# Kernel tuning notes

Hardware: AMD Instinct MI355X
Metric: run time of the kernel (lower is better)

The kernel has to match this reference:

```python
import jax, jax.numpy as jnp
import numpy as np

# Config (mirrors CorrLayerDownsample(J=3, L=8, A=1, A_prime=1, M=256, N=256,
# num_channels=1, shift_mode='samec', mask_angles=4)). With samec + 1 channel,
# every pair is 'shifted' (mask index 1) and groups (j1,j2) are contiguous in
# the global moment order, so concatenation reproduces results_storage order.
J, L, A, M, N, NB = 3, 8, 1, 256, 256, 2
MASK_ANGLES = 4
RADII = (1, 2)  # dyadic shift radii (assumed form of create_masks_shift)

def _mask_positions():
    # shift mask 1: origin plus shifts along mask_angles directions at dyadic radii
    pos = {(0, 0)}
    for k in range(MASK_ANGLES):
        th = np.pi * k / MASK_ANGLES
        for r in RADII:
            pos.add((int(round(r * np.cos(th))), int(round(r * np.sin(th)))))
    return sorted(pos)

def _union_flat_idx(h, w):
    # row-major flat indices of the union shift mask at resolution (h, w),
    # matching torch boolean-mask indexing order (mask_downsample + mask_idx_map_1)
    return np.array(sorted(((dx % h) * w + (dy % w)) for dx, dy in _mask_positions()), dtype=np.int64)

UNION_IDX = [_union_flat_idx(M >> j, N >> j) for j in range(J)]
NSHIFT = len(UNION_IDX[0])

# per-(j1,j2) channel gather indices: la = A*L*c + A*l + a = l (A=1, c=0)
# loop order in compute_idx: l1 outer, l2 inner
LA1 = np.repeat(np.arange(L), L)
LA2 = np.tile(np.arange(L), L)

def _spectral_pad(xh, Mn, Nn):
    # zero-pad Fourier representation to (Mn, Nn) -- spectral upsampling
    m, n = xh.shape[-2], xh.shape[-1]
    if (m, n) == (Mn, Nn):
        return xh
    xs = jnp.fft.fftshift(xh, axes=(-2, -1))
    ph, pw = (Mn - m) // 2, (Nn - n) // 2
    pad = [(0, 0)] * (xh.ndim - 2) + [(ph, ph), (pw, pw)]
    xp = jnp.pad(xs, pad)
    return jnp.fft.ifftshift(xp, axes=(-2, -1)) * ((Mn * Nn) / (m * n))

def _forward(xpsi_0, xpsi_1, xpsi_2):
    xs = [xpsi_0, xpsi_1, xpsi_2]
    hats = [jnp.fft.fft2(x.astype(jnp.complex64)) for x in xs]  # [nb, C, h_j, w_j]
    la1 = jnp.asarray(LA1)
    la2 = jnp.asarray(LA2)
    outs = []
    for j1 in range(J):
        h, w = M >> j1, N >> j1
        uidx = jnp.asarray(UNION_IDX[j1])
        h1 = hats[j1][:, la1]  # [nb, P=L*L, h, w]
        for j2 in range(j1, J):
            h2 = hats[j2][:, la2]
            if j2 > j1:
                h2 = _spectral_pad(h2, h, w)  # upsample coarser scale to scale j1
            corr = jnp.fft.ifft2(h1 * jnp.conj(h2)).real  # cross-correlation map
            flat = corr.reshape(corr.shape[0], corr.shape[1], h * w)
            outs.append(flat[:, :, uidx])  # masked downsample: keep shift positions
    return jnp.concatenate(outs, axis=1)  # [nb, total_pairs, NSHIFT]

def setup_inputs():
    key = jax.random.key(0)
    ks = jax.random.split(key, 3)
    return {
        "xpsi_0": jax.random.normal(ks[0], (NB, A * L, M, N), dtype=jnp.float32),
        "xpsi_1": jax.random.normal(ks[1], (NB, A * L, M // 2, N // 2), dtype=jnp.float32),
        "xpsi_2": jax.random.normal(ks[2], (NB, A * L, M // 4, N // 4), dtype=jnp.float32),
    }

def reference(xpsi_0, xpsi_1, xpsi_2):
    return _forward(xpsi_0, xpsi_1, xpsi_2)
```

## Files before the change

### kernel.cpp

```cpp
#include <hip/hip_runtime.h>

#define PI_D 3.14159265358979323846
#define PI_F 3.14159265358979323846f


__device__ inline float rtab_val(int n, int m2, int t) {
  if (t == 0) return 1.0f;
  double th = PI_D * (double)t / (double)n;
  double v = sin(th * (double)(m2 - 1)) / sin(th) + cos(th * (double)m2);
  return (float)(v / (double)m2);
}

__global__ __launch_bounds__(256) void k_front(
    const float* __restrict__ X0, const float* __restrict__ X1,
    const float* __restrict__ X2, float* __restrict__ P1p,
    float* __restrict__ P2p, float* __restrict__ V01, float* __restrict__ V02,
    float* __restrict__ V12, float* __restrict__ T01, float* __restrict__ T02,
    float* __restrict__ T12, float* __restrict__ out) {
  __shared__ float fsm[3840];
  int bid = blockIdx.x;
  int t = threadIdx.x;
  if (bid < 192) {
    const float* X; float* P; int lg, nsp, idx0;
    if (bid < 128) { X = X1; P = P1p; lg = 7; nsp = 8; idx0 = bid; }
    else           { X = X2; P = P2p; lg = 6; nsp = 4; idx0 = bid - 128; }
    int ch = idx0 / nsp, split = idx0 % nsp;
    int n = 1 << lg;
    int total = n * n;
    int chunk = total / nsp;
    int b0 = split * chunk;
    const float* x = X + (size_t)ch * total + b0;
    float s = 0.f;
    for (int i = t; i < chunk; i += 256) {
      int idx = b0 + i;
      float v = x[i];
      s += (((idx >> lg) ^ idx) & 1) ? -v : v;
    }
#pragma unroll
    for (int off = 32; off > 0; off >>= 1) s += __shfl_down(s, off, 64);
    __shared__ float red[4];
    if ((t & 63) == 0) red[t >> 6] = s;
    __syncthreads();
    if (t == 0) P[ch * nsp + split] = red[0] + red[1] + red[2] + red[3];
    return;
  }
  if (bid < 320) {
    int idx = bid - 192;
    int ch = idx >> 3, nxg = (idx & 7) * 16;
    float* Rl = fsm;
    float* Xs = fsm + 256;
    for (int i = t; i < 256; i += 256) Rl[i] = rtab_val(256, 128, i);
    const float4* xch4 =
        (const float4*)(X1 + (size_t)ch * 16384 + (size_t)nxg * 128);
    for (int i = t; i < 512; i += 256) ((float4*)Xs)[i] = xch4[i];
    __syncthreads();
    if (idx == 0)
      for (int i = t; i < 256; i += 256) T01[i] = Rl[i];
    float* vch = V01 + (size_t)ch * 128 * 256;
    for (int i = t; i < 2048; i += 256) {
      int r = i >> 7, k = i & 127;
      vch[(size_t)(nxg + r) * 256 + 2 * k] = Xs[r * 128 + k];
    }
    int cid = t & 63, wq = t >> 6;
    int m0 = 2 * cid + 1, m1 = 2 * cid + 129;
    float acc[4][2];
#pragma unroll
    for (int r = 0; r < 4; ++r) { acc[r][0] = 0.f; acc[r][1] = 0.f; }
    for (int ny = 0; ny < 128; ++ny) {
      float r0 = Rl[(m0 - 2 * ny) & 255];
      float r1 = Rl[(m1 - 2 * ny) & 255];
#pragma unroll
      for (int r = 0; r < 4; ++r) {
        float xv = Xs[(4 * wq + r) * 128 + ny];
        acc[r][0] += xv * r0;
        acc[r][1] += xv * r1;
      }
    }
#pragma unroll
    for (int r = 0; r < 4; ++r) {
      vch[(size_t)(nxg + 4 * wq + r) * 256 + m0] = acc[r][0];
      vch[(size_t)(nxg + 4 * wq + r) * 256 + m1] = acc[r][1];
    }
    return;
  }
  if (bid < 512) {
    int vbid = bid - 320;
    const float* X = X2; float* V;
    int n1, n2, s, ch, nxg, colh;
    if (vbid < 128) {
      V = V02; n1 = 256; n2 = 64; s = 4;
      ch = vbid >> 3; nxg = ((vbid >> 1) & 3) * 16; colh = vbid & 1;
    } else {
      int w = vbid - 128;
      V = V12; n1 = 128; n2 = 64; s = 2;
      ch = w >> 2; nxg = (w & 3) * 16; colh = 0;
    }
    float* Rl = fsm;
    float* Xs = fsm + 256;
    for (int i = t; i < n1; i += 256) Rl[i] = rtab_val(n1, n2, i);
    const float4* xch4 =
        (const float4*)(X + (size_t)ch * n2 * n2 + (size_t)nxg * n2);
    int nx4 = (16 * n2) >> 2;
    for (int i = t; i < nx4; i += 256) ((float4*)Xs)[i] = xch4[i];
    __syncthreads();
    if (vbid == 0)
      for (int i = t; i < 256; i += 256) T02[i] = Rl[i];
    if (vbid == 128)
      for (int i = t; i < 128; i += 256) T12[i] = Rl[i];
    int myq = (t & 63) + colh * 128;
    int nxq = t >> 6;
    int mask = n1 - 1;
    float acc[4][2];
#pragma unroll
    for (int r = 0; r < 4; ++r)
#pragma unroll
      for (int c = 0; c < 2; ++c) acc[r][c] = 0.f;
    for (int ny = 0; ny < n2; ++ny) {
      float xv[4];
#pragma unroll
      for (int r = 0; r < 4; ++r) xv[r] = Xs[(4 * nxq + r) * n2 + ny];
#pragma unroll
      for (int c = 0; c < 2; ++c) {
        float rv = Rl[(myq + 64 * c - s * ny) & mask];
#pragma unroll
        for (int r = 0; r < 4; ++r) acc[r][c] += xv[r] * rv;
      }
    }
    float* vch = V + (size_t)ch * n2 * n1;
#pragma unroll
    for (int r = 0; r < 4; ++r)
      for (int c = 0; c < 2; ++c)
        vch[(size_t)(nxg + 4 * nxq + r) * n1 + myq + 64 * c] = acc[r][c];
    return;
  }
  int lane = t & 63;
  int wv = t >> 6;
  float accC[8][7];
#pragma unroll
  for (int i = 0; i < 8; ++i)
#pragma unroll
    for (int p = 0; p < 7; ++p) accC[i][p] = 0.f;
  int w = bid - 512;
  const float* Ab; int loc, lgn1, lgc, base;
  if (w < 256)      { loc = w;       Ab = X0; lgn1 = 8; lgc = 4; base = 0;   }
  else if (w < 384) { loc = w - 256; Ab = X1; lgn1 = 7; lgc = 3; base = 192; }
  else              { loc = w - 384; Ab = X2; lgn1 = 6; lgc = 2; base = 320; }
  int n1 = 1 << lgn1;
  int mask = n1 - 1;
  int n1sq = n1 * n1;
  int chunk = loc & ((1 << lgc) - 1);
  int bl2 = loc >> lgc;
  int b = bl2 >> 3, l2 = bl2 & 7;
  const float* A1 = Ab + (size_t)(b * 8) * n1sq;
  const float* A2 = Ab + (size_t)(b * 8 + l2) * n1sq;
  int lgtpr = lgn1 - 2;
  int tpr = 1 << lgtpr;
  int rif = 256 >> lgtpr;
  int rid = t >> lgtpr;
  int cid2 = t & (tpr - 1);
  int ty = cid2 * 4;
  int tym = (ty - 4) & mask;
  for (int rr = 0; rr < 16; rr += rif) {
    int row = chunk * 16 + rr + rid;
    const float* r0 = A2 + (size_t)row * n1;
    const float* r1 = A2 + (size_t)((row - 1) & mask) * n1;
    const float* r2 = A2 + (size_t)((row - 2) & mask) * n1;
    const float* r3 = A2 + (size_t)((row + 1) & mask) * n1;
    float4 a0 = *(const float4*)(r0 + tym);
    float4 b0 = *(const float4*)(r0 + ty);
    float4 a1 = *(const float4*)(r1 + tym);
    float4 b1 = *(const float4*)(r1 + ty);
    float4 b2 = *(const float4*)(r2 + ty);
    float4 a3 = *(const float4*)(r3 + tym);
    float4 b3 = *(const float4*)(r3 + ty);
    const float* rA = A1 + (size_t)row * n1 + ty;
#pragma unroll
    for (int l1 = 0; l1 < 8; ++l1) {
      float4 xv = *(const float4*)(rA + (size_t)l1 * n1sq);
      accC[l1][0] += xv.x * b0.x + xv.y * b0.y + xv.z * b0.z + xv.w * b0.w;
      accC[l1][1] += xv.x * a0.w + xv.y * b0.x + xv.z * b0.y + xv.w * b0.z;
      accC[l1][2] += xv.x * a0.z + xv.y * a0.w + xv.z * b0.x + xv.w * b0.y;
      accC[l1][3] += xv.x * b1.x + xv.y * b1.y + xv.z * b1.z + xv.w * b1.w;
      accC[l1][4] += xv.x * a1.w + xv.y * b1.x + xv.z * b1.y + xv.w * b1.z;
      accC[l1][5] += xv.x * b2.x + xv.y * b2.y + xv.z * b2.z + xv.w * b2.w;
      accC[l1][6] += xv.x * a3.w + xv.y * b3.x + xv.z * b3.y + xv.w * b3.z;
    }
  }
  float* sh = fsm;
  float* af = &accC[0][0];
#pragma unroll
  for (int j = 0; j < 56; ++j) {
    float v = af[j];
    v += __shfl_down(v, 32, 64);
    v += __shfl_down(v, 16, 64);
    af[j] = v;
  }
  __syncthreads();
  if (lane < 16) {
    float* rowp = sh + (wv * 16 + lane) * 60;
#pragma unroll
    for (int j = 0; j < 14; ++j)
      *(float4*)&rowp[4 * j] =
          make_float4(af[4 * j], af[4 * j + 1], af[4 * j + 2], af[4 * j + 3]);
  }
  __syncthreads();
  if (t < 224) {
    int v = t >> 2, q = t & 3;
    float s2 = 0.f;
#pragma unroll
    for (int i = 0; i < 16; ++i) s2 += sh[(q * 16 + i) * 60 + v];
    s2 += __shfl_down(s2, 2, 64);
    s2 += __shfl_down(s2, 1, 64);
    if (q == 0) {
      int l1o = v / 7, p = v % 7;
      atomicAdd(&out[((size_t)b * 384 + base + l1o * 8 + l2) * 7 + p], s2);
    }
  }
}

__global__ __launch_bounds__(256) void k_main(const float* __restrict__ X0,
                                              const float* __restrict__ X1,
                                              const float* __restrict__ V01,
                                              const float* __restrict__ V02,
                                              const float* __restrict__ V12,
                                              const float* __restrict__ P1p,
                                              const float* __restrict__ P2p,
                                              const float* __restrict__ T01,
                                              const float* __restrict__ T02,
                                              const float* __restrict__ T12,
                                              float* __restrict__ out) {
  __shared__ float sRl[256];
  __shared__ float sh[4864];
  __shared__ float Vs[2][2048];
  int u = blockIdx.x;
  int t = threadIdx.x;
  int lane = t & 63;
  int wv = t >> 6;

  const float* V; const float* Pp; const float* A1b; const float* T;
  int n1, n2, s, ch, chunk, nsp, lgn1, base; float inv;
  if (u < 256) {
    V = V01; Pp = P1p; nsp = 8; A1b = X0; n1 = 256; n2 = 128; s = 2;
    inv = 1.f / 16384.f; ch = u >> 4; chunk = u & 15; lgn1 = 8; base = 64;
    T = T01;
  } else if (u < 512) {
    int w = u - 256;
    V = V02; Pp = P2p; nsp = 4; A1b = X0; n1 = 256; n2 = 64; s = 4;
    inv = 1.f / 4096.f; ch = w >> 4; chunk = w & 15; lgn1 = 8; base = 128;
    T = T02;
  } else {
    int w = u - 512;
    V = V12; Pp = P2p; nsp = 4; A1b = X1; n1 = 128; n2 = 64; s = 2;
    inv = 1.f / 4096.f; ch = w >> 3; chunk = w & 7; lgn1 = 7; base = 256;
    T = T12;
  }
  int mask = n1 - 1;
  for (int i = t; i < n1; i += 256) sRl[i] = T[i];
  int mxg = chunk * 16;
  int b = ch >> 3, l2 = ch & 7;
  const float* vch = V + (size_t)ch * n2 * n1;
  float Pv = 0.f;
  for (int i = 0; i < nsp; ++i) Pv += Pp[ch * nsp + i];
  float a = PI_F / (float)s;
  int per = 2 * s;

  if (n1 == 256) {
    if (s == 2) {
      for (int i = t; i < 640; i += 256) {
        int rl = 2 * (i >> 6), c4 = (i & 63) * 4;
        int mx = (mxg - 2 + rl) & 255;
        *(float4*)&sh[rl * 256 + c4] =
            *(const float4*)(vch + (size_t)(mx >> 1) * 256 + c4);
      }
    } else {
      for (int i = t; i < 320; i += 256) {
        int rl = 2 + 4 * (i >> 6), c4 = (i & 63) * 4;
        int mx = (mxg - 2 + rl) & 255;
        *(float4*)&sh[rl * 256 + c4] =
            *(const float4*)(vch + (size_t)(mx >> 2) * 256 + c4);
      }
    }
  } else {
    for (int i = t; i < 320; i += 256) {
      int rl = 2 * (i >> 5), c4 = (i & 31) * 4;
      int mx = (mxg - 2 + rl) & 127;
      *(float4*)&sh[rl * 128 + c4] =
          *(const float4*)(vch + (size_t)(mx >> 1) * 128 + c4);
    }
  }

  int nr, rls[4];
  if (s == 2) {
    if (wv == 0)      { nr = 3; rls[0] = 1;  rls[1] = 3;  rls[2] = 5;  rls[3] = 1; }
    else if (wv == 1) { nr = 2; rls[0] = 7;  rls[1] = 9;  rls[2] = 7;  rls[3] = 7; }
    else if (wv == 2) { nr = 2; rls[0] = 11; rls[1] = 13; rls[2] = 11; rls[3] = 11; }
    else              { nr = 2; rls[0] = 15; rls[1] = 17; rls[2] = 15; rls[3] = 15; }
  } else {
    if (wv == 0)      { nr = 4; rls[0] = 0;  rls[1] = 1;  rls[2] = 3;  rls[3] = 4; }
    else if (wv == 1) { nr = 4; rls[0] = 5;  rls[1] = 7;  rls[2] = 8;  rls[3] = 9; }
    else if (wv == 2) { nr = 3; rls[0] = 11; rls[1] = 12; rls[2] = 13; rls[3] = 11; }
    else              { nr = 3; rls[0] = 15; rls[1] = 16; rls[2] = 17; rls[3] = 15; }
  }
  int bj[4];
#pragma unroll
  for (int j = 0; j < 4; ++j) bj[j] = (mxg - 2 + rls[j]) & mask;

  const float4* vp4 = (const float4*)vch;
  if (n1 == 256) {
    int ntl = n2 >> 3;
    for (int i = t; i < 512; i += 256) ((float4*)Vs[0])[i] = vp4[i];
    __syncthreads();
    float4 acc[4];
#pragma unroll
    for (int j = 0; j < 4; ++j) acc[j] = make_float4(0.f, 0.f, 0.f, 0.f);
    for (int tl = 0; tl < ntl; ++tl) {
      float4 stg0, stg1;
      bool has = (tl + 1 < ntl);
      if (has) {
        stg0 = vp4[(size_t)(tl + 1) * 512 + t];
        stg1 = vp4[(size_t)(tl + 1) * 512 + 256 + t];
      }
      const float* Vc = Vs[tl & 1];
      int tb = tl * 8;
#pragma unroll
      for (int kk = 0; kk < 8; ++kk) {
        float4 vv = *(const float4*)&Vc[kk * 256 + 4 * lane];
        int ss = s * (tb + kk);
#pragma unroll
        for (int j = 0; j < 4; ++j)
          if (j < nr) {
            float rv = sRl[(bj[j] - ss) & 255];
            acc[j].x += rv * vv.x;
            acc[j].y += rv * vv.y;
            acc[j].z += rv * vv.z;
            acc[j].w += rv * vv.w;
          }
      }
      if (has) {
        float4* d = (float4*)Vs[(tl & 1) ^ 1];
        d[t] = stg0;
        d[256 + t] = stg1;
      }
      __syncthreads();
    }
    float smy[4];
#pragma unroll
    for (int j = 0; j < 4; ++j)
      smy[j] = sinf(a * (float)((4 * lane + j) & (per - 1)));
#pragma unroll
    for (int j = 0; j < 4; ++j)
      if (j < nr) {
        float q = inv * sinf(a * (float)(bj[j] & (per - 1))) * Pv;
        float4 o = acc[j];
        o.x -= q * smy[0];
        o.y -= q * smy[1];
        o.z -= q * smy[2];
        o.w -= q * smy[3];
        *(float4*)&sh[rls[j] * 256 + 4 * lane] = o;
      }
  } else {
    for (int i = t; i < 256; i += 256) ((float4*)Vs[0])[i] = vp4[i];
    __syncthreads();
    float2 acc[4];
#pragma unroll
    for (int j = 0; j < 4; ++j) acc[j] = make_float2(0.f, 0.f);
    for (int tl = 0; tl < 8; ++tl) {
      float4 stg0;
      bool has = (tl + 1 < 8);
      if (has) stg0 = vp4[(size_t)(tl + 1) * 256 + t];
      const float* Vc = Vs[tl & 1];
      int tb = tl * 8;
#pragma unroll
      for (int kk = 0; kk < 8; ++kk) {
        float2 vv = *(const float2*)&Vc[kk * 128 + 2 * lane];
        int ss = 2 * (tb + kk);
#pragma unroll
        for (int j = 0; j < 4; ++j)
          if (j < nr) {
            float rv = sRl[(bj[j] - ss) & 127];
            acc[j].x += rv * vv.x;
            acc[j].y += rv * vv.y;
          }
      }
      if (has) ((float4*)Vs[(tl & 1) ^ 1])[t] = stg0;
      __syncthreads();
    }
    const float a2 = PI_F * 0.5f;
    float smy0 = sinf(a2 * (float)((2 * lane) & 3));
    float smy1 = sinf(a2 * (float)((2 * lane + 1) & 3));
#pragma unroll
    for (int j = 0; j < 4; ++j)
      if (j < nr) {
        float q = inv * sinf(a2 * (float)(bj[j] & 3)) * Pv;
        float2 o = acc[j];
        o.x -= q * smy0;
        o.y -= q * smy1;
        *(float2*)&sh[rls[j] * 128 + 2 * lane] = o;
      }
  }
  __syncthreads();

  float accC[8][7];
#pragma unroll
  for (int i = 0; i < 8; ++i)
#pragma unroll
    for (int p = 0; p < 7; ++p) accC[i][p] = 0.f;
  int lgtpr = lgn1 - 2;
  int tpr = 1 << lgtpr;
  int rif = 256 >> lgtpr;
  int rid = t >> lgtpr;
  int cid2 = t & (tpr - 1);
  int ty = cid2 * 4;
  int tym = (ty - 4) & mask;
  int n1sq = n1 * n1;
  const float* A1 = A1b + (size_t)(b * 8) * n1sq;
  for (int rr = 0; rr < 16; rr += rif) {
    int ri = rr + rid;
    const float* r0 = &sh[(ri + 2) * n1];
    const float* r1 = &sh[(ri + 1) * n1];
    const float* r2 = &sh[ri * n1];
    const float* r3 = &sh[(ri + 3) * n1];
    float4 a0 = *(const float4*)(r0 + tym);
    float4 b0 = *(const float4*)(r0 + ty);
    float4 a1 = *(const float4*)(r1 + tym);
    float4 b1 = *(const float4*)(r1 + ty);
    float4 b2 = *(const float4*)(r2 + ty);
    float4 a3 = *(const float4*)(r3 + tym);
    float4 b3 = *(const float4*)(r3 + ty);
    const float* rA = A1 + (size_t)(mxg + ri) * n1 + ty;
#pragma unroll
    for (int l1 = 0; l1 < 8; ++l1) {
      float4 xv = *(const float4*)(rA + (size_t)l1 * n1sq);
      accC[l1][0] += xv.x * b0.x + xv.y * b0.y + xv.z * b0.z + xv.w * b0.w;
      accC[l1][1] += xv.x * a0.w + xv.y * b0.x + xv.z * b0.y + xv.w * b0.z;
      accC[l1][2] += xv.x * a0.z + xv.y * a0.w + xv.z * b0.x + xv.w * b0.y;
      accC[l1][3] += xv.x * b1.x + xv.y * b1.y + xv.z * b1.z + xv.w * b1.w;
      accC[l1][4] += xv.x * a1.w + xv.y * b1.x + xv.z * b1.y + xv.w * b1.z;
      accC[l1][5] += xv.x * b2.x + xv.y * b2.y + xv.z * b2.z + xv.w * b2.w;
      accC[l1][6] += xv.x * a3.w + xv.y * b3.x + xv.z * b3.y + xv.w * b3.z;
    }
  }

  float* af = &accC[0][0];
#pragma unroll
  for (int j = 0; j < 56; ++j) {
    float v = af[j];
    v += __shfl_down(v, 32, 64);
    v += __shfl_down(v, 16, 64);
    af[j] = v;
  }
  __syncthreads();
  if (lane < 16) {
    float* rowp = sh + (wv * 16 + lane) * 60;
#pragma unroll
    for (int j = 0; j < 14; ++j)
      *(float4*)&rowp[4 * j] =
          make_float4(af[4 * j], af[4 * j + 1], af[4 * j + 2], af[4 * j + 3]);
  }
  __syncthreads();
  if (t < 224) {
    int v = t >> 2, q = t & 3;
    float s2 = 0.f;
#pragma unroll
    for (int i = 0; i < 16; ++i) s2 += sh[(q * 16 + i) * 60 + v];
    s2 += __shfl_down(s2, 2, 64);
    s2 += __shfl_down(s2, 1, 64);
    if (q == 0) {
      int l1o = v / 7, p = v % 7;
      atomicAdd(&out[((size_t)b * 384 + base + l1o * 8 + l2) * 7 + p], s2);
    }
  }
}

extern "C" void kernel_launch(void* const* d_in, const int* in_sizes, int n_in,
                              void* d_out, int out_size, void* d_ws, size_t ws_size,
                              hipStream_t stream) {
  const float* X0 = (const float*)d_in[0];
  const float* X1 = (const float*)d_in[1];
  const float* X2 = (const float*)d_in[2];
  float* out = (float*)d_out;
  float* ws = (float*)d_ws;

  float* V01 = ws + 2359296;
  float* V02 = ws + 2883584;
  float* V12 = ws + 3145728;
  float* P1p = ws + 3276800;
  float* P2p = ws + 3276928;
  float* T01 = ws + 3276992;
  float* T02 = ws + 3277248;
  float* T12 = ws + 3277504;

  hipMemsetAsync(d_out, 0, (size_t)out_size, stream);
  k_front<<<960, 256, 0, stream>>>(X0, X1, X2, P1p, P2p, V01, V02, V12, T01,
                                   T02, T12, out);
  k_main<<<640, 256, 0, stream>>>(X0, X1, V01, V02, V12, P1p, P2p, T01, T02,
                                  T12, out);
}
```

Measured before the change: 96.27 us.

## Move same-scale correlation blocks into main kernel and zero output in-kernel

The same-scale direct-correlation blocks (448 of them) move from the front kernel into the main kernel, which grows from 640 to 1088 blocks. The front kernel shrinks to the V/P precompute plus one extra block that zeroes the output buffer, replacing the separate hipMemsetAsync. This drops one memset launch and shortens the critical-path front kernel, and the front kernel's shared buffer shrinks. The risk is a heavier, more register-hungry main kernel and less overlap between the independent correlation work and the precompute stage.

Result: slower. 107.2 us (+11.4%).

```diff
diff --git a/kernel.cpp b/kernel.cpp
--- a/kernel.cpp
+++ b/kernel.cpp
@@ -17,9 +17,13 @@
     float* __restrict__ P2p, float* __restrict__ V01, float* __restrict__ V02,
     float* __restrict__ V12, float* __restrict__ T01, float* __restrict__ T02,
     float* __restrict__ T12, float* __restrict__ out) {
-  __shared__ float fsm[3840];
+  __shared__ float fsm[2304];
   int bid = blockIdx.x;
   int t = threadIdx.x;
+  if (bid == 512) {
+    for (int i = t; i < 5376; i += 256) out[i] = 0.f;
+    return;
+  }
   if (bid < 192) {
     const float* X; float* P; int lg, nsp, idx0;
     if (bid < 128) { X = X1; P = P1p; lg = 7; nsp = 8; idx0 = bid; }
@@ -83,7 +87,7 @@
     }
     return;
   }
-  if (bid < 512) {
+  {
     int vbid = bid - 320;
     const float* X = X2; float* V;
     int n1, n2, s, ch, nxg, colh;
@@ -131,95 +135,12 @@
     for (int r = 0; r < 4; ++r)
       for (int c = 0; c < 2; ++c)
         vch[(size_t)(nxg + 4 * nxq + r) * n1 + myq + 64 * c] = acc[r][c];
-    return;
-  }
-  int lane = t & 63;
-  int wv = t >> 6;
-  float accC[8][7];
-#pragma unroll
-  for (int i = 0; i < 8; ++i)
-#pragma unroll
-    for (int p = 0; p < 7; ++p) accC[i][p] = 0.f;
-  int w = bid - 512;
-  const float* Ab; int loc, lgn1, lgc, base;
-  if (w < 256)      { loc = w;       Ab = X0; lgn1 = 8; lgc = 4; base = 0;   }
-  else if (w < 384) { loc = w - 256; Ab = X1; lgn1 = 7; lgc = 3; base = 192; }
-  else              { loc = w - 384; Ab = X2; lgn1 = 6; lgc = 2; base = 320; }
-  int n1 = 1 << lgn1;
-  int mask = n1 - 1;
-  int n1sq = n1 * n1;
-  int chunk = loc & ((1 << lgc) - 1);
-  int bl2 = loc >> lgc;
-  int b = bl2 >> 3, l2 = bl2 & 7;
-  const float* A1 = Ab + (size_t)(b * 8) * n1sq;
-  const float* A2 = Ab + (size_t)(b * 8 + l2) * n1sq;
-  int lgtpr = lgn1 - 2;
-  int tpr = 1 << lgtpr;
-  int rif = 256 >> lgtpr;
-  int rid = t >> lgtpr;
-  int cid2 = t & (tpr - 1);
-  int ty = cid2 * 4;
-  int tym = (ty - 4) & mask;
-  for (int rr = 0; rr < 16; rr += rif) {
-    int row = chunk * 16 + rr + rid;
-    const float* r0 = A2 + (size_t)row * n1;
-    const float* r1 = A2 + (size_t)((row - 1) & mask) * n1;
-    const float* r2 = A2 + (size_t)((row - 2) & mask) * n1;
-    const float* r3 = A2 + (size_t)((row + 1) & mask) * n1;
-    float4 a0 = *(const float4*)(r0 + tym);
-    float4 b0 = *(const float4*)(r0 + ty);
-    float4 a1 = *(const float4*)(r1 + tym);
-    float4 b1 = *(const float4*)(r1 + ty);
-    float4 b2 = *(const float4*)(r2 + ty);
-    float4 a3 = *(const float4*)(r3 + tym);
-    float4 b3 = *(const float4*)(r3 + ty);
-    const float* rA = A1 + (size_t)row * n1 + ty;
-#pragma unroll
-    for (int l1 = 0; l1 < 8; ++l1) {
-      float4 xv = *(const float4*)(rA + (size_t)l1 * n1sq);
-      accC[l1][0] += xv.x * b0.x + xv.y * b0.y + xv.z * b0.z + xv.w * b0.w;
-      accC[l1][1] += xv.x * a0.w + xv.y * b0.x + xv.z * b0.y + xv.w * b0.z;
-      accC[l1][2] += xv.x * a0.z + xv.y * a0.w + xv.z * b0.x + xv.w * b0.y;
-      accC[l1][3] += xv.x * b1.x + xv.y * b1.y + xv.z * b1.z + xv.w * b1.w;
-      accC[l1][4] += xv.x * a1.w + xv.y * b1.x + xv.z * b1.y + xv.w * b1.z;
-      accC[l1][5] += xv.x * b2.x + xv.y * b2.y + xv.z * b2.z + xv.w * b2.w;
-      accC[l1][6] += xv.x * a3.w + xv.y * b3.x + xv.z * b3.y + xv.w * b3.z;
-    }
-  }
-  float* sh = fsm;
-  float* af = &accC[0][0];
-#pragma unroll
-  for (int j = 0; j < 56; ++j) {
-    float v = af[j];
-    v += __shfl_down(v, 32, 64);
-    v += __shfl_down(v, 16, 64);
-    af[j] = v;
-  }
-  __syncthreads();
-  if (lane < 16) {
-    float* rowp = sh + (wv * 16 + lane) * 60;
-#pragma unroll
-    for (int j = 0; j < 14; ++j)
-      *(float4*)&rowp[4 * j] =
-          make_float4(af[4 * j], af[4 * j + 1], af[4 * j + 2], af[4 * j + 3]);
-  }
-  __syncthreads();
-  if (t < 224) {
-    int v = t >> 2, q = t & 3;
-    float s2 = 0.f;
-#pragma unroll
-    for (int i = 0; i < 16; ++i) s2 += sh[(q * 16 + i) * 60 + v];
-    s2 += __shfl_down(s2, 2, 64);
-    s2 += __shfl_down(s2, 1, 64);
-    if (q == 0) {
-      int l1o = v / 7, p = v % 7;
-      atomicAdd(&out[((size_t)b * 384 + base + l1o * 8 + l2) * 7 + p], s2);
-    }
   }
 }
 
 __global__ __launch_bounds__(256) void k_main(const float* __restrict__ X0,
                                               const float* __restrict__ X1,
+                                              const float* __restrict__ X2,
                                               const float* __restrict__ V01,
                                               const float* __restrict__ V02,
                                               const float* __restrict__ V12,
@@ -237,207 +158,259 @@
   int lane = t & 63;
   int wv = t >> 6;
 
-  const float* V; const float* Pp; const float* A1b; const float* T;
-  int n1, n2, s, ch, chunk, nsp, lgn1, base; float inv;
-  if (u < 256) {
-    V = V01; Pp = P1p; nsp = 8; A1b = X0; n1 = 256; n2 = 128; s = 2;
-    inv = 1.f / 16384.f; ch = u >> 4; chunk = u & 15; lgn1 = 8; base = 64;
-    T = T01;
-  } else if (u < 512) {
-    int w = u - 256;
-    V = V02; Pp = P2p; nsp = 4; A1b = X0; n1 = 256; n2 = 64; s = 4;
-    inv = 1.f / 4096.f; ch = w >> 4; chunk = w & 15; lgn1 = 8; base = 128;
-    T = T02;
-  } else {
-    int w = u - 512;
-    V = V12; Pp = P2p; nsp = 4; A1b = X1; n1 = 128; n2 = 64; s = 2;
-    inv = 1.f / 4096.f; ch = w >> 3; chunk = w & 7; lgn1 = 7; base = 256;
-    T = T12;
-  }
-  int mask = n1 - 1;
-  for (int i = t; i < n1; i += 256) sRl[i] = T[i];
-  int mxg = chunk * 16;
-  int b = ch >> 3, l2 = ch & 7;
-  const float* vch = V + (size_t)ch * n2 * n1;
-  float Pv = 0.f;
-  for (int i = 0; i < nsp; ++i) Pv += Pp[ch * nsp + i];
-  float a = PI_F / (float)s;
-  int per = 2 * s;
-
-  if (n1 == 256) {
-    if (s == 2) {
-      for (int i = t; i < 640; i += 256) {
-        int rl = 2 * (i >> 6), c4 = (i & 63) * 4;
-        int mx = (mxg - 2 + rl) & 255;
-        *(float4*)&sh[rl * 256 + c4] =
-            *(const float4*)(vch + (size_t)(mx >> 1) * 256 + c4);
+  float accC[8][7];
+#pragma unroll
+  for (int i = 0; i < 8; ++i)
+#pragma unroll
+    for (int p = 0; p < 7; ++p) accC[i][p] = 0.f;
+
+  int b, l2, base;
+
+  if (u < 640) {
+    const float* V; const float* Pp; const float* A1b; const float* T;
+    int n1, n2, s, ch, chunk, nsp, lgn1; float inv;
+    if (u < 256) {
+      V = V01; Pp = P1p; nsp = 8; A1b = X0; n1 = 256; n2 = 128; s = 2;
+      inv = 1.f / 16384.f; ch = u >> 4; chunk = u & 15; lgn1 = 8; base = 64;
+      T = T01;
+    } else if (u < 512) {
+      int w = u - 256;
+      V = V02; Pp = P2p; nsp = 4; A1b = X0; n1 = 256; n2 = 64; s = 4;
+      inv = 1.f / 4096.f; ch = w >> 4; chunk = w & 15; lgn1 = 8; base = 128;
+      T = T02;
+    } else {
+      int w = u - 512;
+      V = V12; Pp = P2p; nsp = 4; A1b = X1; n1 = 128; n2 = 64; s = 2;
+      inv = 1.f / 4096.f; ch = w >> 3; chunk = w & 7; lgn1 = 7; base = 256;
+      T = T12;
+    }
+    int mask = n1 - 1;
+    for (int i = t; i < n1; i += 256) sRl[i] = T[i];
+    int mxg = chunk * 16;
+    b = ch >> 3; l2 = ch & 7;
+    const float* vch = V + (size_t)ch * n2 * n1;
+    float Pv = 0.f;
+    for (int i = 0; i < nsp; ++i) Pv += Pp[ch * nsp + i];
+    float a = PI_F / (float)s;
+    int per = 2 * s;
+
+    if (n1 == 256) {
+      if (s == 2) {
+        for (int i = t; i < 640; i += 256) {
+          int rl = 2 * (i >> 6), c4 = (i & 63) * 4;
+          int mx = (mxg - 2 + rl) & 255;
+          *(float4*)&sh[rl * 256 + c4] =
+              *(const float4*)(vch + (size_t)(mx >> 1) * 256 + c4);
+        }
+      } else {
+        for (int i = t; i < 320; i += 256) {
+          int rl = 2 + 4 * (i >> 6), c4 = (i & 63) * 4;
+          int mx = (mxg - 2 + rl) & 255;
+          *(float4*)&sh[rl * 256 + c4] =
+              *(const float4*)(vch + (size_t)(mx >> 2) * 256 + c4);
+        }
       }
     } else {
       for (int i = t; i < 320; i += 256) {
-        int rl = 2 + 4 * (i >> 6), c4 = (i & 63) * 4;
-        int mx = (mxg - 2 + rl) & 255;
-        *(float4*)&sh[rl * 256 + c4] =
-            *(const float4*)(vch + (size_t)(mx >> 2) * 256 + c4);
+        int rl = 2 * (i >> 5), c4 = (i & 31) * 4;
+        int mx = (mxg - 2 + rl) & 127;
+        *(float4*)&sh[rl * 128 + c4] =
+            *(const float4*)(vch + (size_t)(mx >> 1) * 128 + c4);
+      }
+    }
+
+    int nr, rls[4];
+    if (s == 2) {
+      if (wv == 0)      { nr = 3; rls[0] = 1;  rls[1] = 3;  rls[2] = 5;  rls[3] = 1; }
+      else if (wv == 1) { nr = 2; rls[0] = 7;  rls[1] = 9;  rls[2] = 7;  rls[3] = 7; }
+      else if (wv == 2) { nr = 2; rls[0] = 11; rls[1] = 13; rls[2] = 11; rls[3] = 11; }
+      else              { nr = 2; rls[0] = 15; rls[1] = 17; rls[2] = 15; rls[3] = 15; }
+    } else {
+      if (wv == 0)      { nr = 4; rls[0] = 0;  rls[1] = 1;  rls[2] = 3;  rls[3] = 4; }
+      else if (wv == 1) { nr = 4; rls[0] = 5;  rls[1] = 7;  rls[2] = 8;  rls[3] = 9; }
+      else if (wv == 2) { nr = 3; rls[0] = 11; rls[1] = 12; rls[2] = 13; rls[3] = 11; }
+      else              { nr = 3; rls[0] = 15; rls[1] = 16; rls[2] = 17; rls[3] = 15; }
+    }
+    int bj[4];
+#pragma unroll
+    for (int j = 0; j < 4; ++j) bj[j] = (mxg - 2 + rls[j]) & mask;
+
+    const float4* vp4 = (const float4*)vch;
+    if (n1 == 256) {
+      int ntl = n2 >> 3;
+      for (int i = t; i < 512; i += 256) ((float4*)Vs[0])[i] = vp4[i];
+      __syncthreads();
+      float4 acc[4];
+#pragma unroll
+      for (int j = 0; j < 4; ++j) acc[j] = make_float4(0.f, 0.f, 0.f, 0.f);
+      for (int tl = 0; tl < ntl; ++tl) {
+        float4 stg0, stg1;
+        bool has = (tl + 1 < ntl);
+        if (has) {
+          stg0 = vp4[(size_t)(tl + 1) * 512 + t];
+          stg1 = vp4[(size_t)(tl + 1) * 512 + 256 + t];
+        }
+        const float* Vc = Vs[tl & 1];
+        int tb = tl * 8;
+#pragma unroll
+        for (int kk = 0; kk < 8; ++kk) {
+          float4 vv = *(const float4*)&Vc[kk * 256 + 4 * lane];
+          int ss = s * (tb + kk);
+#pragma unroll
+          for (int j = 0; j < 4; ++j)
+            if (j < nr) {
+              float rv = sRl[(bj[j] - ss) & 255];
+              acc[j].x += rv * vv.x;
+              acc[j].y += rv * vv.y;
+              acc[j].z += rv * vv.z;
+              acc[j].w += rv * vv.w;
+            }
+        }
+        if (has) {
+          float4* d = (float4*)Vs[(tl & 1) ^ 1];
+          d[t] = stg0;
+          d[256 + t] = stg1;
+        }
+        __syncthreads();
+      }
+      float smy[4];
+#pragma unroll
+      for (int j = 0; j < 4; ++j)
+        smy[j] = sinf(a * (float)((4 * lane + j) & (per - 1)));
+#pragma unroll
+      for (int j = 0; j < 4; ++j)
+        if (j < nr) {
+          float q = inv * sinf(a * (float)(bj[j] & (per - 1))) * Pv;
+          float4 o = acc[j];
+          o.x -= q * smy[0];
+          o.y -= q * smy[1];
+          o.z -= q * smy[2];
+          o.w -= q * smy[3];
+          *(float4*)&sh[rls[j] * 256 + 4 * lane] = o;
+        }
+    } else {
+      for (int i = t; i < 256; i += 256) ((float4*)Vs[0])[i] = vp4[i];
+      __syncthreads();
+      float2 acc[4];
+#pragma unroll
+      for (int j = 0; j < 4; ++j) acc[j] = make_float2(0.f, 0.f);
+      for (int tl = 0; tl < 8; ++tl) {
+        float4 stg0;
+        bool has = (tl + 1 < 8);
+        if (has) stg0 = vp4[(size_t)(tl + 1) * 256 + t];
+        const float* Vc = Vs[tl & 1];
+        int tb = tl * 8;
+#pragma unroll
+        for (int kk = 0; kk < 8; ++kk) {
+          float2 vv = *(const float2*)&Vc[kk * 128 + 2 * lane];
+          int ss = 2 * (tb + kk);
+#pragma unroll
+          for (int j = 0; j < 4; ++j)
+            if (j < nr) {
+              float rv = sRl[(bj[j] - ss) & 127];
+              acc[j].x += rv * vv.x;
+              acc[j].y += rv * vv.y;
+            }
+        }
+        if (has) ((float4*)Vs[(tl & 1) ^ 1])[t] = stg0;
+        __syncthreads();
+      }
+      const float a2 = PI_F * 0.5f;
+      float smy0 = sinf(a2 * (float)((2 * lane) & 3));
+      float smy1 = sinf(a2 * (float)((2 * lane + 1) & 3));
+#pragma unroll
+      for (int j = 0; j < 4; ++j)
+        if (j < nr) {
+          float q = inv * sinf(a2 * (float)(bj[j] & 3)) * Pv;
+          float2 o = acc[j];
+          o.x -= q * smy0;
+          o.y -= q * smy1;
+          *(float2*)&sh[rls[j] * 128 + 2 * lane] = o;
+        }
+    }
+    __syncthreads();
+
+    int lgtpr = lgn1 - 2;
+    int tpr = 1 << lgtpr;
+    int rif = 256 >> lgtpr;
+    int rid = t >> lgtpr;
+    int cid2 = t & (tpr - 1);
+    int ty = cid2 * 4;
+    int tym = (ty - 4) & mask;
+    int n1sq = n1 * n1;
+    const float* A1 = A1b + (size_t)(b * 8) * n1sq;
+    for (int rr = 0; rr < 16; rr += rif) {
+      int ri = rr + rid;
+      const float* r0 = &sh[(ri + 2) * n1];
+      const float* r1 = &sh[(ri + 1) * n1];
+      const float* r2 = &sh[ri * n1];
+      const float* r3 = &sh[(ri + 3) * n1];
+      float4 a0 = *(const float4*)(r0 + tym);
+      float4 b0 = *(const float4*)(r0 + ty);
+      float4 a1 = *(const float4*)(r1 + tym);
+      float4 b1 = *(const float4*)(r1 + ty);
+      float4 b2 = *(const float4*)(r2 + ty);
+      float4 a3 = *(const float4*)(r3 + tym);
+      float4 b3 = *(const float4*)(r3 + ty);
+      const float* rA = A1 + (size_t)(mxg + ri) * n1 + ty;
+#pragma unroll
+      for (int l1 = 0; l1 < 8; ++l1) {
+        float4 xv = *(const float4*)(rA + (size_t)l1 * n1sq);
+        accC[l1][0] += xv.x * b0.x + xv.y * b0.y + xv.z * b0.z + xv.w * b0.w;
+        accC[l1][1] += xv.x * a0.w + xv.y * b0.x + xv.z * b0.y + xv.w * b0.z;
+        accC[l1][2] += xv.x * a0.z + xv.y * a0.w + xv.z * b0.x + xv.w * b0.y;
+        accC[l1][3] += xv.x * b1.x + xv.y * b1.y + xv.z * b1.z + xv.w * b1.w;
+        accC[l1][4] += xv.x * a1.w + xv.y * b1.x + xv.z * b1.y + xv.w * b1.z;
+        accC[l1][5] += xv.x * b2.x + xv.y * b2.y + xv.z * b2.z + xv.w * b2.w;
+        accC[l1][6] += xv.x * a3.w + xv.y * b3.x + xv.z * b3.y + xv.w * b3.z;
       }
     }
   } else {
-    for (int i = t; i < 320; i += 256) {
-      int rl = 2 * (i >> 5), c4 = (i & 31) * 4;
-      int mx = (mxg - 2 + rl) & 127;
-      *(float4*)&sh[rl * 128 + c4] =
-          *(const float4*)(vch + (size_t)(mx >> 1) * 128 + c4);
-    }
-  }
-
-  int nr, rls[4];
-  if (s == 2) {
-    if (wv == 0)      { nr = 3; rls[0] = 1;  rls[1] = 3;  rls[2] = 5;  rls[3] = 1; }
-    else if (wv == 1) { nr = 2; rls[0] = 7;  rls[1] = 9;  rls[2] = 7;  rls[3] = 7; }
-    else if (wv == 2) { nr = 2; rls[0] = 11; rls[1] = 13; rls[2] = 11; rls[3] = 11; }
-    else              { nr = 2; rls[0] = 15; rls[1] = 17; rls[2] = 15; rls[3] = 15; }
-  } else {
-    if (wv == 0)      { nr = 4; rls[0] = 0;  rls[1] = 1;  rls[2] = 3;  rls[3] = 4; }
-    else if (wv == 1) { nr = 4; rls[0] = 5;  rls[1] = 7;  rls[2] = 8;  rls[3] = 9; }
-    else if (wv == 2) { nr = 3; rls[0] = 11; rls[1] = 12; rls[2] = 13; rls[3] = 11; }
-    else              { nr = 3; rls[0] = 15; rls[1] = 16; rls[2] = 17; rls[3] = 15; }
-  }
-  int bj[4];
-#pragma unroll
-  for (int j = 0; j < 4; ++j) bj[j] = (mxg - 2 + rls[j]) & mask;
-
-  const float4* vp4 = (const float4*)vch;
-  if (n1 == 256) {
-    int ntl = n2 >> 3;
-    for (int i = t; i < 512; i += 256) ((float4*)Vs[0])[i] = vp4[i];
-    __syncthreads();
-    float4 acc[4];
-#pragma unroll
-    for (int j = 0; j < 4; ++j) acc[j] = make_float4(0.f, 0.f, 0.f, 0.f);
-    for (int tl = 0; tl < ntl; ++tl) {
-      float4 stg0, stg1;
-      bool has = (tl + 1 < ntl);
-      if (has) {
-        stg0 = vp4[(size_t)(tl + 1) * 512 + t];
-        stg1 = vp4[(size_t)(tl + 1) * 512 + 256 + t];
-      }
-      const float* Vc = Vs[tl & 1];
-      int tb = tl * 8;
-#pragma unroll
-      for (int kk = 0; kk < 8; ++kk) {
-        float4 vv = *(const float4*)&Vc[kk * 256 + 4 * lane];
-        int ss = s * (tb + kk);
-#pragma unroll
-        for (int j = 0; j < 4; ++j)
-          if (j < nr) {
-            float rv = sRl[(bj[j] - ss) & 255];
-            acc[j].x += rv * vv.x;
-            acc[j].y += rv * vv.y;
-            acc[j].z += rv * vv.z;
-            acc[j].w += rv * vv.w;
-          }
-      }
-      if (has) {
-        float4* d = (float4*)Vs[(tl & 1) ^ 1];
-        d[t] = stg0;
-        d[256 + t] = stg1;
-      }
-      __syncthreads();
-    }
-    float smy[4];
-#pragma unroll
-    for (int j = 0; j < 4; ++j)
-      smy[j] = sinf(a * (float)((4 * lane + j) & (per - 1)));
-#pragma unroll
-    for (int j = 0; j < 4; ++j)
-      if (j < nr) {
-        float q = inv * sinf(a * (float)(bj[j] & (per - 1))) * Pv;
-        float4 o = acc[j];
-        o.x -= q * smy[0];
-        o.y -= q * smy[1];
-        o.z -= q * smy[2];
-        o.w -= q * smy[3];
-        *(float4*)&sh[rls[j] * 256 + 4 * lane] = o;
-      }
-  } else {
-    for (int i = t; i < 256; i += 256) ((float4*)Vs[0])[i] = vp4[i];
-    __syncthreads();
-    float2 acc[4];
-#pragma unroll
-    for (int j = 0; j < 4; ++j) acc[j] = make_float2(0.f, 0.f);
-    for (int tl = 0; tl < 8; ++tl) {
-      float4 stg0;
-      bool has = (tl + 1 < 8);
-      if (has) stg0 = vp4[(size_t)(tl + 1) * 256 + t];
-      const float* Vc = Vs[tl & 1];
-      int tb = tl * 8;
-#pragma unroll
-      for (int kk = 0; kk < 8; ++kk) {
-        float2 vv = *(const float2*)&Vc[kk * 128 + 2 * lane];
-        int ss = 2 * (tb + kk);
-#pragma unroll
-        for (int j = 0; j < 4; ++j)
-          if (j < nr) {
-            float rv = sRl[(bj[j] - ss) & 127];
-            acc[j].x += rv * vv.x;
-            acc[j].y += rv * vv.y;
-          }
-      }
-      if (has) ((float4*)Vs[(tl & 1) ^ 1])[t] = stg0;
-      __syncthreads();
-    }
-    const float a2 = PI_F * 0.5f;
-    float smy0 = sinf(a2 * (float)((2 * lane) & 3));
-    float smy1 = sinf(a2 * (float)((2 * lane + 1) & 3));
-#pragma unroll
-    for (int j = 0; j < 4; ++j)
-      if (j < nr) {
-        float q = inv * sinf(a2 * (float)(bj[j] & 3)) * Pv;
-        float2 o = acc[j];
-        o.x -= q * smy0;
-        o.y -= q * smy1;
-        *(float2*)&sh[rls[j] * 128 + 2 * lane] = o;
-      }
-  }
-  __syncthreads();
-
-  float accC[8][7];
-#pragma unroll
-  for (int i = 0; i < 8; ++i)
-#pragma unroll
-    for (int p = 0; p < 7; ++p) accC[i][p] = 0.f;
-  int lgtpr = lgn1 - 2;
-  int tpr = 1 << lgtpr;
-  int rif = 256 >> lgtpr;
-  int rid = t >> lgtpr;
-  int cid2 = t & (tpr - 1);
-  int ty = cid2 * 4;
-  int tym = (ty - 4) & mask;
-  int n1sq = n1 * n1;
-  const float* A1 = A1b + (size_t)(b * 8) * n1sq;
-  for (int rr = 0; rr < 16; rr += rif) {
-    int ri = rr + rid;
-    const float* r0 = &sh[(ri + 2) * n1];
-    const float* r1 = &sh[(ri + 1) * n1];
-    const float* r2 = &sh[ri * n1];
-    const float* r3 = &sh[(ri + 3) * n1];
-    float4 a0 = *(const float4*)(r0 + tym);
-    float4 b0 = *(const float4*)(r0 + ty);
-    float4 a1 = *(const float4*)(r1 + tym);
-    float4 b1 = *(const float4*)(r1 + ty);
-    float4 b2 = *(const float4*)(r2 + ty);
-    float4 a3 = *(const float4*)(r3 + tym);
-    float4 b3 = *(const float4*)(r3 + ty);
-    const float* rA = A1 + (size_t)(mxg + ri) * n1 + ty;
-#pragma unroll
-    for (int l1 = 0; l1 < 8; ++l1) {
-      float4 xv = *(const float4*)(rA + (size_t)l1 * n1sq);
-      accC[l1][0] += xv.x * b0.x + xv.y * b0.y + xv.z * b0.z + xv.w * b0.w;
-      accC[l1][1] += xv.x * a0.w + xv.y * b0.x + xv.z * b0.y + xv.w * b0.z;
-      accC[l1][2] += xv.x * a0.z + xv.y * a0.w + xv.z * b0.x + xv.w * b0.y;
-      accC[l1][3] += xv.x * b1.x + xv.y * b1.y + xv.z * b1.z + xv.w * b1.w;
-      accC[l1][4] += xv.x * a1.w + xv.y * b1.x + xv.z * b1.y + xv.w * b1.z;
-      accC[l1][5] += xv.x * b2.x + xv.y * b2.y + xv.z * b2.z + xv.w * b2.w;
-      accC[l1][6] += xv.x * a3.w + xv.y * b3.x + xv.z * b3.y + xv.w * b3.z;
+    int w = u - 640;
+    const float* Ab; int loc, lgn1, lgc;
+    if (w < 256)      { loc = w;       Ab = X0; lgn1 = 8; lgc = 4; base = 0;   }
+    else if (w < 384) { loc = w - 256; Ab = X1; lgn1 = 7; lgc = 3; base = 192; }
+    else              { loc = w - 384; Ab = X2; lgn1 = 6; lgc = 2; base = 320; }
+    int n1 = 1 << lgn1;
+    int mask = n1 - 1;
+    int n1sq = n1 * n1;
+    int chunk = loc & ((1 << lgc) - 1);
+    int bl2 = loc >> lgc;
+    b = bl2 >> 3; l2 = bl2 & 7;
+    const float* A1 = Ab + (size_t)(b * 8) * n1sq;
+    const float* A2 = Ab + (size_t)(b * 8 + l2) * n1sq;
+    int lgtpr = lgn1 - 2;
+    int tpr = 1 << lgtpr;
+    int rif = 256 >> lgtpr;
+    int rid = t >> lgtpr;
+    int cid2 = t & (tpr - 1);
+    int ty = cid2 * 4;
+    int tym = (ty - 4) & mask;
+    for (int rr = 0; rr < 16; rr += rif) {
+      int row = chunk * 16 + rr + rid;
+      const float* r0 = A2 + (size_t)row * n1;
+      const float* r1 = A2 + (size_t)((row - 1) & mask) * n1;
+      const float* r2 = A2 + (size_t)((row - 2) & mask) * n1;
+      const float* r3 = A2 + (size_t)((row + 1) & mask) * n1;
+      float4 a0 = *(const float4*)(r0 + tym);
+      float4 b0 = *(const float4*)(r0 + ty);
+      float4 a1 = *(const float4*)(r1 + tym);
+      float4 b1 = *(const float4*)(r1 + ty);
+      float4 b2 = *(const float4*)(r2 + ty);
+      float4 a3 = *(const float4*)(r3 + tym);
+      float4 b3 = *(const float4*)(r3 + ty);
+      const float* rA = A1 + (size_t)row * n1 + ty;
+#pragma unroll
+      for (int l1 = 0; l1 < 8; ++l1) {
+        float4 xv = *(const float4*)(rA + (size_t)l1 * n1sq);
+        accC[l1][0] += xv.x * b0.x + xv.y * b0.y + xv.z * b0.z + xv.w * b0.w;
+        accC[l1][1] += xv.x * a0.w + xv.y * b0.x + xv.z * b0.y + xv.w * b0.z;
+        accC[l1][2] += xv.x * a0.z + xv.y * a0.w + xv.z * b0.x + xv.w * b0.y;
+        accC[l1][3] += xv.x * b1.x + xv.y * b1.y + xv.z * b1.z + xv.w * b1.w;
+        accC[l1][4] += xv.x * a1.w + xv.y * b1.x + xv.z * b1.y + xv.w * b1.z;
+        accC[l1][5] += xv.x * b2.x + xv.y * b2.y + xv.z * b2.z + xv.w * b2.w;
+        accC[l1][6] += xv.x * a3.w + xv.y * b3.x + xv.z * b3.y + xv.w * b3.z;
+      }
     }
   }
 
@@ -490,9 +463,8 @@
   float* T02 = ws + 3277248;
   float* T12 = ws + 3277504;
 
-  hipMemsetAsync(d_out, 0, (size_t)out_size, stream);
-  k_front<<<960, 256, 0, stream>>>(X0, X1, X2, P1p, P2p, V01, V02, V12, T01,
+  k_front<<<513, 256, 0, stream>>>(X0, X1, X2, P1p, P2p, V01, V02, V12, T01,
                                    T02, T12, out);
-  k_main<<<640, 256, 0, stream>>>(X0, X1, V01, V02, V12, P1p, P2p, T01, T02,
-                                  T12, out);
+  k_main<<<1088, 256, 0, stream>>>(X0, X1, X2, V01, V02, V12, P1p, P2p, T01,
+                                   T02, T12, out);
 }
```
